# Performance work log

Measured on AMD Instinct MI355X. Metric: run time of the kernel, lower is better.

Reference implementation:

```python
import jax, jax.numpy as jnp
import numpy as np

N_EMBED = 1024
N_HEADS = 16
HEAD_DIM = N_EMBED // N_HEADS


def setup_inputs() -> dict:
    key = jax.random.key(0)
    ks = jax.random.split(key, 5)
    x = jax.random.normal(ks[0], (4, 2048, N_EMBED), dtype=jnp.float32)
    # Linear params (torch nn.Linear: y = x @ W.T + b); store W as [in, out]
    s = 1.0 / np.sqrt(N_EMBED)
    W_attn = jax.random.uniform(ks[1], (N_EMBED, 3 * N_EMBED), minval=-s, maxval=s, dtype=jnp.float32)
    b_attn = jax.random.uniform(ks[2], (3 * N_EMBED,), minval=-s, maxval=s, dtype=jnp.float32)
    W_proj = jax.random.uniform(ks[3], (N_EMBED, N_EMBED), minval=-s, maxval=s, dtype=jnp.float32)
    b_proj = jax.random.uniform(ks[4], (N_EMBED,), minval=-s, maxval=s, dtype=jnp.float32)
    return {"x": x, "W_attn": W_attn, "b_attn": b_attn, "W_proj": W_proj, "b_proj": b_proj}


def reference(x, W_attn, b_attn, W_proj, b_proj):
    B, L, D = x.shape
    H, Hd = N_HEADS, HEAD_DIM
    qkv = x @ W_attn + b_attn  # [B, L, 3D]
    q, k, v = jnp.split(qkv, 3, axis=-1)
    q = q.reshape(B, L, H, Hd).transpose(0, 2, 1, 3)  # [B, H, L, Hd]
    k = k.reshape(B, L, H, Hd).transpose(0, 2, 1, 3)
    v = v.reshape(B, L, H, Hd).transpose(0, 2, 1, 3)
    scores = jnp.einsum('bhqd,bhkd->bhqk', q, k) / jnp.sqrt(jnp.float32(Hd))
    causal = jnp.tril(jnp.ones((L, L), dtype=bool))
    scores = jnp.where(causal[None, None], scores, -jnp.inf)
    probs = jax.nn.softmax(scores.astype(jnp.float32), axis=-1).astype(x.dtype)
    o = jnp.einsum('bhqk,bhkd->bhqd', probs, v)  # [B, H, L, Hd]
    o = o.transpose(0, 2, 1, 3).reshape(B, L, D)
    return o @ W_proj + b_proj
```

## Files before the change

### kernel.cpp

```cpp
#include <hip/hip_runtime.h>


typedef __attribute__((ext_vector_type(8))) short short8;
typedef __attribute__((ext_vector_type(4))) short s16x4;
typedef __attribute__((ext_vector_type(4))) float f32x4;

#define DEVI __device__ __forceinline__

constexpr int NE = 1024, NH = 16, NB = 4, L = 2048;
constexpr int M = NB * L;
constexpr int KD = 1024;

DEVI unsigned f2bf(float f) {
    union { float f; unsigned u; } v; v.f = f;
    unsigned u = v.u;
    u += 0x7fffu + ((u >> 16) & 1u);
    return u >> 16;
}
DEVI unsigned pack_bf2(float lo, float hi) {
    union { float f; unsigned u; } a, b; a.f = lo; b.f = hi;
    return ((a.u + 0x8000u) >> 16) | ((b.u + 0x8000u) & 0xffff0000u);
}

typedef const __attribute__((address_space(1))) void* gas_t;
typedef __attribute__((address_space(3))) void* las_t;
DEVI void gl_lds16(const void* g, void* l) {
    __builtin_amdgcn_global_load_lds((gas_t)g, (las_t)l, 16, 0, 0);
}

__global__ void k_f32_to_bf16(const float* __restrict__ in,
                              unsigned short* __restrict__ out, int n8) {
    int i = blockIdx.x * blockDim.x + threadIdx.x;
    if (i >= n8) return;
    const float4* p = (const float4*)in + (size_t)i * 2;
    float4 a = p[0], b = p[1];
    short8 r;
    r[0] = f2bf(a.x); r[1] = f2bf(a.y); r[2] = f2bf(a.z); r[3] = f2bf(a.w);
    r[4] = f2bf(b.x); r[5] = f2bf(b.y); r[6] = f2bf(b.z); r[7] = f2bf(b.w);
    ((short8*)out)[i] = r;
}

__global__ void k_transpose_bf16(const float* __restrict__ in,
                                 unsigned short* __restrict__ out, int R, int C) {
    __shared__ float t[32][33];
    int x = blockIdx.x * 32 + threadIdx.x;
    int y0 = blockIdx.y * 32;
#pragma unroll
    for (int i = 0; i < 4; i++)
        t[threadIdx.y + 8 * i][threadIdx.x] = in[(size_t)(y0 + threadIdx.y + 8 * i) * C + x];
    __syncthreads();
    int xo = y0 + threadIdx.x;
    int yo = blockIdx.x * 32 + threadIdx.y;
#pragma unroll
    for (int i = 0; i < 4; i++)
        out[(size_t)(yo + 8 * i) * R + xo] = f2bf(t[threadIdx.x][threadIdx.y + 8 * i]);
}

template <int MODE>
__global__ __launch_bounds__(256, 4)
void k_gemm(const unsigned short* __restrict__ A,
            const unsigned short* __restrict__ Bt,
            const float* __restrict__ bias,
            unsigned short* __restrict__ Qb,
            unsigned short* __restrict__ Kb,
            unsigned short* __restrict__ Vt,
            float* __restrict__ out) {
    constexpr int NBN  = (MODE == 0) ? 24 : 8;
    constexpr int GRID = (MODE == 0) ? 768 : 512;
    constexpr int REPS = (MODE == 0) ? 2 : 1;

    __shared__ alignas(16) short As[128 * 64];
    __shared__ alignas(16) short Bs[128 * 64];
    const int tid = threadIdx.x;
    const int lane = tid & 63, wid = tid >> 6;
    const int quad = lane >> 4, l16 = lane & 15;
    const int wm = (wid >> 1) * 64, wn = (wid & 1) * 64;

    const int srow = lane >> 3;
    const int gseg = (lane & 7) ^ srow;

    const int p = (int)blockIdx.x;
    const int ps = (p & 7) * (GRID / 8) + (p >> 3);

    for (int rep = 0; rep < REPS; rep++) {
        const int t = ps + rep * GRID;
        const int n0 = (t % NBN) * 128;
        const int m0 = (t / NBN) * 128;

        f32x4 acc[4][4] = {};

        for (int kk = 0; kk < KD; kk += 64) {
            __syncthreads();
#pragma unroll
            for (int c = 0; c < 4; c++) {
                const int rbase = c * 32 + wid * 8;
                gl_lds16(&A[(size_t)(m0 + rbase + srow) * KD + kk + gseg * 8], &As[rbase * 64]);
                gl_lds16(&Bt[(size_t)(n0 + rbase + srow) * KD + kk + gseg * 8], &Bs[rbase * 64]);
            }
            __syncthreads();
#pragma unroll
            for (int kc = 0; kc < 2; kc++) {
                short8 af[4], bf[4];
#pragma unroll
                for (int tt = 0; tt < 4; tt++) {
                    const int Ra = wm + tt * 16 + l16;
                    af[tt] = *(const short8*)&As[Ra * 64 + (((kc * 4 + quad) ^ (Ra & 7)) * 8)];
                    const int Rb = wn + tt * 16 + l16;
                    bf[tt] = *(const short8*)&Bs[Rb * 64 + (((kc * 4 + quad) ^ (Rb & 7)) * 8)];
                }
#pragma unroll
                for (int mt = 0; mt < 4; mt++)
#pragma unroll
                    for (int nt = 0; nt < 4; nt++)
                        acc[mt][nt] = __builtin_amdgcn_mfma_f32_16x16x32_bf16(
                            af[mt], bf[nt], acc[mt][nt], 0, 0, 0);
            }
        }

#pragma unroll
        for (int nt = 0; nt < 4; nt++) {
            const int n = n0 + wn + nt * 16 + l16;
            const float bv = bias[n];
            if (MODE == 0) {
                const int sel = n >> 10;
                const int h = (n & 1023) >> 6;
                const int d = n & 63;
#pragma unroll
                for (int mt = 0; mt < 4; mt++)
#pragma unroll
                    for (int r = 0; r < 4; r++) {
                        const int m = m0 + wm + mt * 16 + quad * 4 + r;
                        const int b = m >> 11, l = m & 2047;
                        const int bh = b * NH + h;
                        const float v = acc[mt][nt][r] + bv;
                        if (sel == 0)      Qb[(size_t)(bh * L + l) * 64 + d] = f2bf(v * 0.125f);
                        else if (sel == 1) Kb[(size_t)(bh * L + l) * 64 + d] = f2bf(v);
                        else               Vt[(size_t)(bh * 64 + d) * L + l] = f2bf(v);
                    }
            } else {
#pragma unroll
                for (int mt = 0; mt < 4; mt++)
#pragma unroll
                    for (int r = 0; r < 4; r++) {
                        const int m = m0 + wm + mt * 16 + quad * 4 + r;
                        out[(size_t)m * NE + n] = acc[mt][nt][r] + bv;
                    }
            }
        }
    }
}

__global__ __launch_bounds__(512, 2)
void k_attn(const unsigned short* __restrict__ Q,
            const unsigned short* __restrict__ Kb,
            const unsigned short* __restrict__ Vt,
            unsigned short* __restrict__ O) {
    __shared__ alignas(16) short smem[32768];
    short* Os = smem;

    const int tid = threadIdx.x;
    const int lane = tid & 63, wid = tid >> 6;
    const int quad = lane >> 4, l16 = lane & 15;
    const int p = (int)blockIdx.x;
    const int bh = p >> 2, pi = p & 3;
    const size_t base = (size_t)bh * L * 64;
    const int b = bh >> 4, h = bh & 15;

    const int srowK = lane >> 3;
    const int gsegK = (lane & 7) ^ srowK;
    const int vrow_off = (lane >> 4);
    const int vseg = lane & 15;

    auto stK = [&](int j, int buf) {
#pragma unroll
        for (int c = 0; c < 2; c++) {
            const int rbase = c * 64 + wid * 8;
            gl_lds16(&Kb[base + (size_t)(j * 128 + rbase + srowK) * 64 + gsegK * 8],
                     &smem[buf * 8192 + rbase * 64]);
        }
    };
    auto stV = [&](int j, int buf) {
#pragma unroll
        for (int c = 0; c < 2; c++) {
            const int rbase = c * 32 + wid * 4;
            const int row = rbase + vrow_off;
            const int gs = vseg ^ (row & 15);
            gl_lds16(&Vt[base + (size_t)row * L + j * 128 + gs * 8],
                     &smem[16384 + buf * 8192 + rbase * 128]);
        }
    };

    for (int half = 0; half < 2; half++) {
        const int qb = half ? pi : 7 - pi;
        const int q0 = qb * 256 + wid * 32;
        const int nkv = 2 * qb + 2;

        __syncthreads();
        stK(0, 0); stV(0, 0);

        short8 qf[2][2];
#pragma unroll
        for (int mt = 0; mt < 2; mt++)
#pragma unroll
            for (int dc = 0; dc < 2; dc++)
                qf[mt][dc] = *(const short8*)&Q[base + (size_t)(q0 + mt * 16 + l16) * 64 + dc * 32 + quad * 8];

        f32x4 o[2][4] = {};
        float lrow[2] = {0.f, 0.f};

        for (int j = 0; j < nkv; j++) {
            asm volatile("s_waitcnt vmcnt(0)" ::: "memory");
            __builtin_amdgcn_s_barrier();
            if (j < nkv - 1) { stK(j + 1, (j + 1) & 1); stV(j + 1, (j + 1) & 1); }

            const short* Ks = &smem[(j & 1) * 8192];
            const short* Vs = &smem[16384 + (j & 1) * 8192];

            const int dmc = 8 * qb + wid - 4 * j;
            int chunks = dmc + 1;
            chunks = chunks < 0 ? 0 : (chunks > 4 ? 4 : chunks);

            for (int kc = 0; kc < chunks; kc++) {
                short8 kf[2][2];
#pragma unroll
                for (int j0 = 0; j0 < 2; j0++)
#pragma unroll
                    for (int dc = 0; dc < 2; dc++) {
                        const int R = kc * 32 + j0 * 16 + l16;
                        kf[j0][dc] = *(const short8*)&Ks[R * 64 + (((dc * 4 + quad) ^ (R & 7)) * 8)];
                    }
                f32x4 st[2][2];
                __builtin_amdgcn_s_setprio(1);
#pragma unroll
                for (int mt = 0; mt < 2; mt++)
#pragma unroll
                    for (int j0 = 0; j0 < 2; j0++) {
                        f32x4 z = {};
                        z = __builtin_amdgcn_mfma_f32_16x16x32_bf16(kf[j0][0], qf[mt][0], z, 0, 0, 0);
                        z = __builtin_amdgcn_mfma_f32_16x16x32_bf16(kf[j0][1], qf[mt][1], z, 0, 0, 0);
                        st[mt][j0] = z;
                    }
                __builtin_amdgcn_s_setprio(0);
                const bool dm = (kc == dmc);
                short8 pb[2];
#pragma unroll
                for (int mt = 0; mt < 2; mt++) {
                    float pe[8];
                    float sum = 0.f;
#pragma unroll
                    for (int j0 = 0; j0 < 2; j0++)
#pragma unroll
                        for (int r = 0; r < 4; r++) {
                            float pv = __expf(st[mt][j0][r]);
                            if (dm) {
                                const int krel = j0 * 16 + quad * 4 + r;
                                const int qrel = mt * 16 + l16;
                                if (krel > qrel) pv = 0.f;
                            }
                            sum += pv;
                            pe[j0 * 4 + r] = pv;
                        }
                    lrow[mt] += sum;
#pragma unroll
                    for (int w = 0; w < 4; w++) {
                        unsigned pk = pack_bf2(pe[2 * w], pe[2 * w + 1]);
                        pb[mt][2 * w] = (short)(pk & 0xffff);
                        pb[mt][2 * w + 1] = (short)(pk >> 16);
                    }
                }
#pragma unroll
                for (int dt = 0; dt < 4; dt++) {
                    const int R2 = dt * 16 + l16;
                    const int s16a = kc * 4 + (quad >> 1);
                    const int off = (quad & 1) * 4;
                    s16x4 lo = *(const s16x4*)&Vs[R2 * 128 + ((s16a ^ l16) * 8) + off];
                    s16x4 hi = *(const s16x4*)&Vs[R2 * 128 + (((s16a + 2) ^ l16) * 8) + off];
                    short8 vf = __builtin_shufflevector(lo, hi, 0, 1, 2, 3, 4, 5, 6, 7);
                    __builtin_amdgcn_s_setprio(1);
#pragma unroll
                    for (int mt = 0; mt < 2; mt++)
                        o[mt][dt] = __builtin_amdgcn_mfma_f32_16x16x32_bf16(
                            vf, pb[mt], o[mt][dt], 0, 0, 0);
                    __builtin_amdgcn_s_setprio(0);
                }
            }
        }

        float inv[2];
#pragma unroll
        for (int mt = 0; mt < 2; mt++) {
            float rs = lrow[mt];
            rs += __shfl_xor(rs, 16);
            rs += __shfl_xor(rs, 32);
            inv[mt] = 1.0f / rs;
        }

        __syncthreads();
#pragma unroll
        for (int mt = 0; mt < 2; mt++) {
            const int ql = wid * 32 + mt * 16 + l16;
#pragma unroll
            for (int dt = 0; dt < 4; dt++) {
                unsigned w0 = f2bf(o[mt][dt][0] * inv[mt]) | (f2bf(o[mt][dt][1] * inv[mt]) << 16);
                unsigned w1 = f2bf(o[mt][dt][2] * inv[mt]) | (f2bf(o[mt][dt][3] * inv[mt]) << 16);
                *(uint2*)&Os[ql * 72 + dt * 16 + quad * 4] = make_uint2(w0, w1);
            }
        }
        __syncthreads();
#pragma unroll
        for (int i2 = 0; i2 < 4; i2++) {
            const int id = i2 * 512 + tid;
            const int row = id >> 3, seg = id & 7;
            short8 v = *(const short8*)&Os[row * 72 + seg * 8];
            const int q = qb * 256 + row;
            *(short8*)&O[(size_t)(b * L + q) * NE + h * 64 + seg * 8] = v;
        }
    }
}

extern "C" void kernel_launch(void* const* d_in, const int* in_sizes, int n_in,
                              void* d_out, int out_size, void* d_ws, size_t ws_size,
                              hipStream_t stream) {
    const float* x  = (const float*)d_in[0];
    const float* Wa = (const float*)d_in[1];
    const float* ba = (const float*)d_in[2];
    const float* Wp = (const float*)d_in[3];
    const float* bp = (const float*)d_in[4];
    float* out = (float*)d_out;

    char* ws = (char*)d_ws;
    unsigned short* xb  = (unsigned short*)(ws);
    unsigned short* WaT = (unsigned short*)(ws + (16u << 20));
    unsigned short* WpT = (unsigned short*)(ws + (22u << 20));
    unsigned short* Qb  = (unsigned short*)(ws + (24u << 20));
    unsigned short* Kb  = (unsigned short*)(ws + (40u << 20));
    unsigned short* Vt  = (unsigned short*)(ws + (56u << 20));

    k_f32_to_bf16<<<(M * NE / 8 + 255) / 256, 256, 0, stream>>>(x, xb, M * NE / 8);
    k_transpose_bf16<<<dim3(3 * NE / 32, NE / 32), dim3(32, 8), 0, stream>>>(Wa, WaT, NE, 3 * NE);
    k_transpose_bf16<<<dim3(NE / 32, NE / 32), dim3(32, 8), 0, stream>>>(Wp, WpT, NE, NE);

    k_gemm<0><<<dim3(768), 256, 0, stream>>>(xb, WaT, ba, Qb, Kb, Vt, nullptr);

    unsigned short* Ob = xb;
    k_attn<<<dim3(256), 512, 0, stream>>>(Qb, Kb, Vt, Ob);

    k_gemm<1><<<dim3(512), 256, 0, stream>>>(Ob, WpT, bp, nullptr, nullptr, nullptr, out);
}
```

Baseline: 244.7 us.

## Merge prep kernels into one launch and use 256x128 GEMM tiles with 512 threads

Folds the x conversion and both weight transposes into a single k_prep launch with a block-index dispatch, removing two kernel launches. The GEMM moves from 256-thread 128x128 tiles (with two tiles per block for the QKV GEMM) to 512-thread blocks computing one 256x128 tile, so each B tile is reused across twice as many rows. This raises per-block LDS to 48KB and changes occupancy to 2 blocks per CU. The projection GEMM grid halves to 256 blocks, which may underfill the device.

```diff
diff --git a/kernel.cpp b/kernel.cpp
--- a/kernel.cpp
+++ b/kernel.cpp
@@ -28,36 +28,48 @@
     __builtin_amdgcn_global_load_lds((gas_t)g, (las_t)l, 16, 0, 0);
 }
 
-__global__ void k_f32_to_bf16(const float* __restrict__ in,
-                              unsigned short* __restrict__ out, int n8) {
-    int i = blockIdx.x * blockDim.x + threadIdx.x;
-    if (i >= n8) return;
-    const float4* p = (const float4*)in + (size_t)i * 2;
-    float4 a = p[0], b = p[1];
-    short8 r;
-    r[0] = f2bf(a.x); r[1] = f2bf(a.y); r[2] = f2bf(a.z); r[3] = f2bf(a.w);
-    r[4] = f2bf(b.x); r[5] = f2bf(b.y); r[6] = f2bf(b.z); r[7] = f2bf(b.w);
-    ((short8*)out)[i] = r;
-}
-
-__global__ void k_transpose_bf16(const float* __restrict__ in,
-                                 unsigned short* __restrict__ out, int R, int C) {
-    __shared__ float t[32][33];
-    int x = blockIdx.x * 32 + threadIdx.x;
-    int y0 = blockIdx.y * 32;
+DEVI void transpose_tile(const float* __restrict__ in, unsigned short* __restrict__ out,
+                         int R, int C, int bx, int by, int tid, float* t ) {
+    const int tx = tid & 31, ty = tid >> 5;
+    const int x = bx * 32 + tx;
+    const int y0 = by * 32;
 #pragma unroll
     for (int i = 0; i < 4; i++)
-        t[threadIdx.y + 8 * i][threadIdx.x] = in[(size_t)(y0 + threadIdx.y + 8 * i) * C + x];
+        t[(ty + 8 * i) * 33 + tx] = in[(size_t)(y0 + ty + 8 * i) * C + x];
     __syncthreads();
-    int xo = y0 + threadIdx.x;
-    int yo = blockIdx.x * 32 + threadIdx.y;
+    const int xo = y0 + tx;
+    const int yo = bx * 32 + ty;
 #pragma unroll
     for (int i = 0; i < 4; i++)
-        out[(size_t)(yo + 8 * i) * R + xo] = f2bf(t[threadIdx.x][threadIdx.y + 8 * i]);
+        out[(size_t)(yo + 8 * i) * R + xo] = f2bf(t[tx * 33 + ty + 8 * i]);
+}
+
+__global__ __launch_bounds__(256)
+void k_prep(const float* __restrict__ x, unsigned short* __restrict__ xb,
+            const float* __restrict__ Wa, unsigned short* __restrict__ WaT,
+            const float* __restrict__ Wp, unsigned short* __restrict__ WpT) {
+    __shared__ float t[32 * 33];
+    const int blk = (int)blockIdx.x;
+    const int tid = threadIdx.x;
+    if (blk < 4096) {
+        const int i = blk * 256 + tid;
+        const float4* p = (const float4*)x + (size_t)i * 2;
+        float4 a = p[0], b = p[1];
+        short8 r;
+        r[0] = f2bf(a.x); r[1] = f2bf(a.y); r[2] = f2bf(a.z); r[3] = f2bf(a.w);
+        r[4] = f2bf(b.x); r[5] = f2bf(b.y); r[6] = f2bf(b.z); r[7] = f2bf(b.w);
+        ((short8*)xb)[i] = r;
+    } else if (blk < 4096 + 3072) {
+        const int id = blk - 4096;
+        transpose_tile(Wa, WaT, NE, 3 * NE, id % 96, id / 96, tid, t);
+    } else {
+        const int id = blk - 7168;
+        transpose_tile(Wp, WpT, NE, NE, id % 32, id / 32, tid, t);
+    }
 }
 
 template <int MODE>
-__global__ __launch_bounds__(256, 4)
+__global__ __launch_bounds__(512, 2)
 void k_gemm(const unsigned short* __restrict__ A,
             const unsigned short* __restrict__ Bt,
             const float* __restrict__ bias,
@@ -66,10 +78,9 @@
             unsigned short* __restrict__ Vt,
             float* __restrict__ out) {
     constexpr int NBN  = (MODE == 0) ? 24 : 8;
-    constexpr int GRID = (MODE == 0) ? 768 : 512;
-    constexpr int REPS = (MODE == 0) ? 2 : 1;
-
-    __shared__ alignas(16) short As[128 * 64];
+    constexpr int GRID = (MODE == 0) ? 768 : 256;
+
+    __shared__ alignas(16) short As[256 * 64];
     __shared__ alignas(16) short Bs[128 * 64];
     const int tid = threadIdx.x;
     const int lane = tid & 63, wid = tid >> 6;
@@ -80,72 +91,72 @@
     const int gseg = (lane & 7) ^ srow;
 
     const int p = (int)blockIdx.x;
-    const int ps = (p & 7) * (GRID / 8) + (p >> 3);
-
-    for (int rep = 0; rep < REPS; rep++) {
-        const int t = ps + rep * GRID;
-        const int n0 = (t % NBN) * 128;
-        const int m0 = (t / NBN) * 128;
-
-        f32x4 acc[4][4] = {};
-
-        for (int kk = 0; kk < KD; kk += 64) {
-            __syncthreads();
-#pragma unroll
-            for (int c = 0; c < 4; c++) {
-                const int rbase = c * 32 + wid * 8;
-                gl_lds16(&A[(size_t)(m0 + rbase + srow) * KD + kk + gseg * 8], &As[rbase * 64]);
-                gl_lds16(&Bt[(size_t)(n0 + rbase + srow) * KD + kk + gseg * 8], &Bs[rbase * 64]);
+    const int t = (p & 7) * (GRID / 8) + (p >> 3);
+    const int n0 = (t % NBN) * 128;
+    const int m0 = (t / NBN) * 256;
+
+    f32x4 acc[4][4] = {};
+
+    for (int kk = 0; kk < KD; kk += 64) {
+        __syncthreads();
+#pragma unroll
+        for (int c = 0; c < 4; c++) {
+            const int rbase = (c * 8 + wid) * 8;
+            gl_lds16(&A[(size_t)(m0 + rbase + srow) * KD + kk + gseg * 8], &As[rbase * 64]);
+        }
+#pragma unroll
+        for (int c = 0; c < 2; c++) {
+            const int rbase = (c * 8 + wid) * 8;
+            gl_lds16(&Bt[(size_t)(n0 + rbase + srow) * KD + kk + gseg * 8], &Bs[rbase * 64]);
+        }
+        __syncthreads();
+#pragma unroll
+        for (int kc = 0; kc < 2; kc++) {
+            short8 af[4], bf[4];
+#pragma unroll
+            for (int tt = 0; tt < 4; tt++) {
+                const int Ra = wm + tt * 16 + l16;
+                af[tt] = *(const short8*)&As[Ra * 64 + (((kc * 4 + quad) ^ (Ra & 7)) * 8)];
+                const int Rb = wn + tt * 16 + l16;
+                bf[tt] = *(const short8*)&Bs[Rb * 64 + (((kc * 4 + quad) ^ (Rb & 7)) * 8)];
             }
-            __syncthreads();
-#pragma unroll
-            for (int kc = 0; kc < 2; kc++) {
-                short8 af[4], bf[4];
-#pragma unroll
-                for (int tt = 0; tt < 4; tt++) {
-                    const int Ra = wm + tt * 16 + l16;
-                    af[tt] = *(const short8*)&As[Ra * 64 + (((kc * 4 + quad) ^ (Ra & 7)) * 8)];
-                    const int Rb = wn + tt * 16 + l16;
-                    bf[tt] = *(const short8*)&Bs[Rb * 64 + (((kc * 4 + quad) ^ (Rb & 7)) * 8)];
+#pragma unroll
+            for (int mt = 0; mt < 4; mt++)
+#pragma unroll
+                for (int nt = 0; nt < 4; nt++)
+                    acc[mt][nt] = __builtin_amdgcn_mfma_f32_16x16x32_bf16(
+                        af[mt], bf[nt], acc[mt][nt], 0, 0, 0);
+        }
+    }
+
+#pragma unroll
+    for (int nt = 0; nt < 4; nt++) {
+        const int n = n0 + wn + nt * 16 + l16;
+        const float bv = bias[n];
+        if (MODE == 0) {
+            const int sel = n >> 10;
+            const int h = (n & 1023) >> 6;
+            const int d = n & 63;
+#pragma unroll
+            for (int mt = 0; mt < 4; mt++)
+#pragma unroll
+                for (int r = 0; r < 4; r++) {
+                    const int m = m0 + wm + mt * 16 + quad * 4 + r;
+                    const int b = m >> 11, l = m & 2047;
+                    const int bh = b * NH + h;
+                    const float v = acc[mt][nt][r] + bv;
+                    if (sel == 0)      Qb[(size_t)(bh * L + l) * 64 + d] = f2bf(v * 0.125f);
+                    else if (sel == 1) Kb[(size_t)(bh * L + l) * 64 + d] = f2bf(v);
+                    else               Vt[(size_t)(bh * 64 + d) * L + l] = f2bf(v);
                 }
-#pragma unroll
-                for (int mt = 0; mt < 4; mt++)
-#pragma unroll
-                    for (int nt = 0; nt < 4; nt++)
-                        acc[mt][nt] = __builtin_amdgcn_mfma_f32_16x16x32_bf16(
-                            af[mt], bf[nt], acc[mt][nt], 0, 0, 0);
-            }
-        }
-
-#pragma unroll
-        for (int nt = 0; nt < 4; nt++) {
-            const int n = n0 + wn + nt * 16 + l16;
-            const float bv = bias[n];
-            if (MODE == 0) {
-                const int sel = n >> 10;
-                const int h = (n & 1023) >> 6;
-                const int d = n & 63;
-#pragma unroll
-                for (int mt = 0; mt < 4; mt++)
-#pragma unroll
-                    for (int r = 0; r < 4; r++) {
-                        const int m = m0 + wm + mt * 16 + quad * 4 + r;
-                        const int b = m >> 11, l = m & 2047;
-                        const int bh = b * NH + h;
-                        const float v = acc[mt][nt][r] + bv;
-                        if (sel == 0)      Qb[(size_t)(bh * L + l) * 64 + d] = f2bf(v * 0.125f);
-                        else if (sel == 1) Kb[(size_t)(bh * L + l) * 64 + d] = f2bf(v);
-                        else               Vt[(size_t)(bh * 64 + d) * L + l] = f2bf(v);
-                    }
-            } else {
-#pragma unroll
-                for (int mt = 0; mt < 4; mt++)
-#pragma unroll
-                    for (int r = 0; r < 4; r++) {
-                        const int m = m0 + wm + mt * 16 + quad * 4 + r;
-                        out[(size_t)m * NE + n] = acc[mt][nt][r] + bv;
-                    }
-            }
+        } else {
+#pragma unroll
+            for (int mt = 0; mt < 4; mt++)
+#pragma unroll
+                for (int r = 0; r < 4; r++) {
+                    const int m = m0 + wm + mt * 16 + quad * 4 + r;
+                    out[(size_t)m * NE + n] = acc[mt][nt][r] + bv;
+                }
         }
     }
 }
@@ -336,14 +347,12 @@
     unsigned short* Kb  = (unsigned short*)(ws + (40u << 20));
     unsigned short* Vt  = (unsigned short*)(ws + (56u << 20));
 
-    k_f32_to_bf16<<<(M * NE / 8 + 255) / 256, 256, 0, stream>>>(x, xb, M * NE / 8);
-    k_transpose_bf16<<<dim3(3 * NE / 32, NE / 32), dim3(32, 8), 0, stream>>>(Wa, WaT, NE, 3 * NE);
-    k_transpose_bf16<<<dim3(NE / 32, NE / 32), dim3(32, 8), 0, stream>>>(Wp, WpT, NE, NE);
-
-    k_gemm<0><<<dim3(768), 256, 0, stream>>>(xb, WaT, ba, Qb, Kb, Vt, nullptr);
+    k_prep<<<dim3(8192), 256, 0, stream>>>(x, xb, Wa, WaT, Wp, WpT);
+
+    k_gemm<0><<<dim3(768), 512, 0, stream>>>(xb, WaT, ba, Qb, Kb, Vt, nullptr);
 
     unsigned short* Ob = xb;
     k_attn<<<dim3(256), 512, 0, stream>>>(Qb, Kb, Vt, Ob);
 
-    k_gemm<1><<<dim3(512), 256, 0, stream>>>(Ob, WpT, bp, nullptr, nullptr, nullptr, out);
-}
+    k_gemm<1><<<dim3(256), 512, 0, stream>>>(Ob, WpT, bp, nullptr, nullptr, nullptr, out);
+}
```

Result: slower. 273.1 us (+11.6%).
